# Kernel optimization log

Hardware: AMD Instinct MI355X
Metric: run time of the kernel (lower is better)

The kernel has to match this reference:

```python
import jax, jax.numpy as jnp
import numpy as np

NEG_INF = -1.0e9  # matches the -1e9 mask constant in the torch module


def setup_inputs() -> dict:
    key = jax.random.key(0)
    k1, k2, k3, k4, k5 = jax.random.split(key, 5)
    B, S, D = 8, 2048, 1024
    x = jax.random.normal(k1, (B, S, D), dtype=jnp.float32)
    mask = jax.random.randint(k2, (B, S), 0, 2, dtype=jnp.int32)
    # torch.nn.Linear stores weight as [out_features, in_features]
    scale = 1.0 / np.sqrt(D)
    w_q = jax.random.normal(k3, (D, D), dtype=jnp.float32) * scale
    w_k = jax.random.normal(k4, (D, D), dtype=jnp.float32) * scale
    w_v = jax.random.normal(k5, (D, D), dtype=jnp.float32) * scale
    return {"x": x, "mask": mask, "w_q": w_q, "w_k": w_k, "w_v": w_v}


def reference(x, mask, w_q, w_k, w_v):
    # Linear (no bias): y = x @ W^T
    q = jnp.einsum("bsd,ed->bse", x, w_q)
    k = jnp.einsum("bsd,ed->bse", x, w_k)
    v = jnp.einsum("bsd,ed->bse", x, w_v)
    # raw (unscaled) scores, exactly as in the torch module
    s = jnp.einsum("bqd,bkd->bqk", q, k)  # [B, S, S]
    # dropout p=0.0 -> identity (eval mode); mask added AFTER dropout
    s = s + NEG_INF * mask.astype(s.dtype)[:, None, :]  # broadcast over query dim
    s = jax.nn.softmax(s, axis=-1)
    out = jnp.einsum("bqk,bkd->bqd", s, v)
    return out, s
```

## Files before the change

kernel.cpp:

```cpp
#include <hip/hip_runtime.h>

#define NEG_INF_F (-1.0e9f)

typedef _Float16 f16x8 __attribute__((ext_vector_type(8)));
typedef float f32x4 __attribute__((ext_vector_type(4)));

__device__ inline unsigned short f16_of(float f) {
    _Float16 h = (_Float16)f;
    return __builtin_bit_cast(unsigned short, h);
}
__device__ inline float f32_of(unsigned short u) {
    return (float)__builtin_bit_cast(_Float16, u);
}

__device__ inline void gload16(const unsigned short* g, unsigned short* l) {
    __builtin_amdgcn_global_load_lds(
        (const __attribute__((address_space(1))) unsigned int*)g,
        (__attribute__((address_space(3))) unsigned int*)l, 16, 0, 0);
}

__device__ inline f16x8 frag32(const unsigned short* t, int r, int ch) {
    return *reinterpret_cast<const f16x8*>(&t[r * 32 + (ch ^ ((r >> 1) & 3)) * 8]);
}
__device__ inline f16x8 frag64(const unsigned short* t, int r, int ch) {
    return *reinterpret_cast<const f16x8*>(&t[r * 64 + (ch ^ (r & 7)) * 8]);
}

__device__ inline void stage_256x32(const unsigned short* __restrict__ g0, int ldg, int k0,
                                    unsigned short* qbuf, int w, int lane) {
#pragma unroll
    for (int c = 0; c < 2; ++c) {
        const int r = c * 128 + w * 16 + (lane >> 2);
        const int co = ((lane & 3) ^ ((r >> 1) & 3)) * 8;
        gload16(g0 + (long long)r * ldg + k0 + co, qbuf + (c * 128 + w * 16) * 32);
    }
}
__device__ inline void stage_128x32(const unsigned short* __restrict__ g0, int ldg, int k0,
                                    unsigned short* qbuf, int w, int lane) {
    const int r = w * 16 + (lane >> 2);
    const int co = ((lane & 3) ^ ((r >> 1) & 3)) * 8;
    gload16(g0 + (long long)r * ldg + k0 + co, qbuf + (w * 16) * 32);
}

template <int OMODE>
__global__ __launch_bounds__(512, 2) void gemm2(
    const unsigned short* __restrict__ Ah_g, const unsigned short* __restrict__ Al_g,
    long long strideA, int lda,
    const unsigned short* __restrict__ Bh_g, long long strideB, int ldb,
    unsigned short* __restrict__ Ch, long long strideC, int ldc, int K)
{
    constexpr int BUF = 16384;
    const int gx = gridDim.x, gy = gridDim.y;
    int bid = blockIdx.x + gx * (blockIdx.y + gy * blockIdx.z);
    const int nwg = gx * gy * gridDim.z;
    bid = (bid & 7) * (nwg >> 3) + (bid >> 3);
    const int bx = bid % gx;
    const int by = (bid / gx) % gy;
    const int b  = bid / (gx * gy);

    const int tid = threadIdx.x;
    const int w = tid >> 6, lane = tid & 63;
    const int wr = w & 1, wc = w >> 1;
    const int lr = lane & 15, lg = lane >> 4;
    const int rowBase = bx * 128;
    const int colBase = by * 256;

    __shared__ unsigned short smem[32768];

    const unsigned short* Ah0 = Ah_g + (long long)b * strideA + (long long)rowBase * lda;
    const unsigned short* Al0 = Al_g + (long long)b * strideA + (long long)rowBase * lda;
    const unsigned short* Bh0 = Bh_g + (long long)b * strideB + (long long)colBase * ldb;

    f32x4 acc[4][4] = {};
    const int NT = K / 32;

    stage_128x32(Ah0, lda, 0, smem, w, lane);
    stage_128x32(Al0, lda, 0, smem + 4096, w, lane);
    stage_256x32(Bh0, ldb, 0, smem + 8192, w, lane);
    __syncthreads();

    for (int kt = 0; kt < NT; ++kt) {
        const unsigned short* cbuf = smem + (kt & 1) * BUF;
        if (kt + 1 < NT) {
            unsigned short* nbuf = smem + ((kt + 1) & 1) * BUF;
            const int k1 = (kt + 1) * 32;
            stage_128x32(Ah0, lda, k1, nbuf, w, lane);
            stage_128x32(Al0, lda, k1, nbuf + 4096, w, lane);
            stage_256x32(Bh0, ldb, k1, nbuf + 8192, w, lane);
        }
        const unsigned short* tAh = cbuf;
        const unsigned short* tAl = cbuf + 4096;
        const unsigned short* tB  = cbuf + 8192;
        f16x8 ah[4], al[4], bh[4];
#pragma unroll
        for (int i = 0; i < 4; ++i) {
            const int r = wr * 64 + i * 16 + lr;
            ah[i] = frag32(tAh, r, lg);
            al[i] = frag32(tAl, r, lg);
        }
#pragma unroll
        for (int j = 0; j < 4; ++j)
            bh[j] = frag32(tB, wc * 64 + j * 16 + lr, lg);
#pragma unroll
        for (int i = 0; i < 4; ++i)
#pragma unroll
            for (int j = 0; j < 4; ++j) {
                f32x4 a = acc[i][j];
                a = __builtin_amdgcn_mfma_f32_16x16x32_f16(ah[i], bh[j], a, 0, 0, 0);
                a = __builtin_amdgcn_mfma_f32_16x16x32_f16(al[i], bh[j], a, 0, 0, 0);
                acc[i][j] = a;
            }
        __syncthreads();
    }

    __syncthreads();
    float* stg = reinterpret_cast<float*>(smem) + w * 2048;
    const int colg0 = colBase + wc * 64;
#pragma unroll
    for (int rnd = 0; rnd < 2; ++rnd) {
        const int rowg0 = rowBase + wr * 64 + rnd * 32;
#pragma unroll
        for (int ii = 0; ii < 2; ++ii)
#pragma unroll
            for (int j = 0; j < 4; ++j)
#pragma unroll
                for (int r2 = 0; r2 < 4; ++r2)
                    stg[(ii * 16 + lg * 4 + r2) * 64 + j * 16 + lr] = acc[rnd * 2 + ii][j][r2];

#pragma unroll
        for (int t = 0; t < 8; ++t) {
            const int idx = t * 256 + lane * 4;
            const int r = idx >> 6, c = idx & 63;
            const float4 v = *reinterpret_cast<const float4*>(&stg[idx]);
            ushort4 h;
            h.x = f16_of(v.x); h.y = f16_of(v.y);
            h.z = f16_of(v.z); h.w = f16_of(v.w);
            *reinterpret_cast<ushort4*>(
                &Ch[(long long)b * strideC + (long long)(rowg0 + r) * ldc + colg0 + c]) = h;
        }
    }
}

__device__ inline void stage_ktile1(
    const unsigned short* __restrict__ Ah0, int lda,
    const unsigned short* __restrict__ Bh0, int ldb,
    int k0, unsigned short* buf, int w, int lane)
{
#pragma unroll
    for (int c = 0; c < 4; ++c) {
        const int r = c * 64 + w * 8 + (lane >> 3);
        const int co = ((lane & 7) ^ (r & 7)) * 8;
        const int lb = (c * 64 + w * 8) * 64;
        gload16(Ah0 + (long long)r * lda + k0 + co, buf + lb);
        gload16(Bh0 + (long long)r * ldb + k0 + co, buf + 16384 + lb);
    }
}

template <int OMODE>
__global__ __launch_bounds__(512, 2) void mfma_gemm1(
    const unsigned short* __restrict__ Ah_g, long long strideA, int lda,
    const unsigned short* __restrict__ Bh_g, long long strideB, int ldb,
    float* __restrict__ Cf, unsigned short* __restrict__ Ch,
    long long strideC, int ldc, int K,
    const int* __restrict__ mask, long long strideMask)
{
    const int b = blockIdx.z;
    const int tid = threadIdx.x;
    const int w = tid >> 6, lane = tid & 63;
    const int wr = w >> 2, wc = w & 3;
    const int lr = lane & 15, lg = lane >> 4;
    const int rowBase = blockIdx.x * 256;
    const int colBase = blockIdx.y * 256;

    __shared__ unsigned short smem[65536];

    const unsigned short* Ah0 = Ah_g + (long long)b * strideA + (long long)rowBase * lda;
    const unsigned short* Bh0 = Bh_g + (long long)b * strideB + (long long)colBase * ldb;

    f32x4 acc[8][4] = {};
    const int NT = K / 64;

    stage_ktile1(Ah0, lda, Bh0, ldb, 0, smem, w, lane);
    __syncthreads();

    for (int kt = 0; kt < NT; ++kt) {
        const unsigned short* cbuf = smem + (kt & 1) * 32768;
        if (kt + 1 < NT)
            stage_ktile1(Ah0, lda, Bh0, ldb, (kt + 1) * 64,
                         smem + ((kt + 1) & 1) * 32768, w, lane);

        const unsigned short* tA = cbuf;
        const unsigned short* tB = cbuf + 16384;
        f16x8 bh[8];
#pragma unroll
        for (int j = 0; j < 4; ++j)
#pragma unroll
            for (int ks = 0; ks < 2; ++ks)
                bh[j * 2 + ks] = frag64(tB, wc * 64 + j * 16 + lr, ks * 4 + lg);
#pragma unroll
        for (int ih = 0; ih < 2; ++ih) {
            f16x8 ah[8];
#pragma unroll
            for (int f = 0; f < 4; ++f)
#pragma unroll
                for (int ks = 0; ks < 2; ++ks)
                    ah[f * 2 + ks] = frag64(tA, wr * 128 + ih * 64 + f * 16 + lr, ks * 4 + lg);
#pragma unroll
            for (int f = 0; f < 4; ++f)
#pragma unroll
                for (int j = 0; j < 4; ++j) {
                    f32x4 a = acc[ih * 4 + f][j];
                    a = __builtin_amdgcn_mfma_f32_16x16x32_f16(ah[f * 2 + 0], bh[j * 2 + 0], a, 0, 0, 0);
                    a = __builtin_amdgcn_mfma_f32_16x16x32_f16(ah[f * 2 + 1], bh[j * 2 + 1], a, 0, 0, 0);
                    acc[ih * 4 + f][j] = a;
                }
        }
        __syncthreads();
    }

    __syncthreads();
    float* stg = reinterpret_cast<float*>(smem) + w * 2048;
    const int colg0 = colBase + wc * 64;
#pragma unroll
    for (int rnd = 0; rnd < 4; ++rnd) {
        const int rowg0 = rowBase + wr * 128 + rnd * 32;
#pragma unroll
        for (int ii = 0; ii < 2; ++ii)
#pragma unroll
            for (int j = 0; j < 4; ++j)
#pragma unroll
                for (int r2 = 0; r2 < 4; ++r2)
                    stg[(ii * 16 + lg * 4 + r2) * 64 + j * 16 + lr] = acc[rnd * 2 + ii][j][r2];

        if constexpr (OMODE == 0) {
#pragma unroll
            for (int t = 0; t < 8; ++t) {
                const int idx = t * 256 + lane * 4;
                const int r = idx >> 6, c = idx & 63;
                float4 v = *reinterpret_cast<const float4*>(&stg[idx]);
                const int colg = colg0 + c;
                if (mask != nullptr) {
                    const int4 mv = *reinterpret_cast<const int4*>(
                        &mask[(long long)b * strideMask + colg]);
                    v.x += NEG_INF_F * (float)mv.x;
                    v.y += NEG_INF_F * (float)mv.y;
                    v.z += NEG_INF_F * (float)mv.z;
                    v.w += NEG_INF_F * (float)mv.w;
                }
                *reinterpret_cast<float4*>(
                    &Cf[(long long)b * strideC + (long long)(rowg0 + r) * ldc + colg]) = v;
            }
        } else {
            const int b2 = rowg0 >> 11;
            const int s0 = rowg0 & 2047;
            const int colg = colg0 + lane;
            alignas(16) unsigned short u[32];
#pragma unroll
            for (int rr = 0; rr < 32; ++rr) u[rr] = f16_of(stg[rr * 64 + lane]);
            unsigned short* vp = Ch + (long long)b2 * (1024LL * 2048)
                               + (long long)colg * 2048 + s0;
#pragma unroll
            for (int q = 0; q < 4; ++q)
                *reinterpret_cast<uint4*>(vp + q * 8) =
                    *reinterpret_cast<const uint4*>(&u[q * 8]);
        }
        __syncthreads();
    }
}

__global__ __launch_bounds__(256) void split2_kernel(
    const float* __restrict__ in, unsigned short* __restrict__ hi,
    unsigned short* __restrict__ lo, long long n)
{
    for (long long i = ((long long)blockIdx.x * 256 + threadIdx.x) * 4; i < n;
         i += (long long)gridDim.x * 256 * 4) {
        float4 v = *reinterpret_cast<const float4*>(&in[i]);
        ushort4 h, l;
        h.x = f16_of(v.x); l.x = f16_of(v.x - f32_of(h.x));
        h.y = f16_of(v.y); l.y = f16_of(v.y - f32_of(h.y));
        h.z = f16_of(v.z); l.z = f16_of(v.z - f32_of(h.z));
        h.w = f16_of(v.w); l.w = f16_of(v.w - f32_of(h.w));
        *reinterpret_cast<ushort4*>(&hi[i]) = h;
        *reinterpret_cast<ushort4*>(&lo[i]) = l;
    }
}

__global__ __launch_bounds__(256) void tsplit_kernel(
    const float* __restrict__ in, unsigned short* __restrict__ hi,
    unsigned short* __restrict__ lo, int N)
{
    __shared__ float tile[64][65];
    const int bi = blockIdx.x * 64;
    const int bj = blockIdx.y * 64;
    const int t = threadIdx.x;
    const int c4 = (t & 15) * 4;
    const int r0 = (t >> 4) * 4;
#pragma unroll
    for (int rr = 0; rr < 4; ++rr) {
        float4 v = *reinterpret_cast<const float4*>(
            &in[(long long)(bi + r0 + rr) * N + bj + c4]);
        tile[r0 + rr][c4 + 0] = v.x;
        tile[r0 + rr][c4 + 1] = v.y;
        tile[r0 + rr][c4 + 2] = v.z;
        tile[r0 + rr][c4 + 3] = v.w;
    }
    __syncthreads();
    const int oc  = t >> 2;
    const int or0 = (t & 3) * 16;
    alignas(16) unsigned short uh[16], ul[16];
#pragma unroll
    for (int e = 0; e < 16; ++e) {
        const float f = tile[or0 + e][oc];
        const unsigned short h = f16_of(f);
        uh[e] = h;
        ul[e] = f16_of(f - f32_of(h));
    }
    unsigned short* hp = hi + (long long)(bj + oc) * N + bi + or0;
    unsigned short* lp = lo + (long long)(bj + oc) * N + bi + or0;
    *reinterpret_cast<uint4*>(hp)     = *reinterpret_cast<const uint4*>(&uh[0]);
    *reinterpret_cast<uint4*>(hp + 8) = *reinterpret_cast<const uint4*>(&uh[8]);
    *reinterpret_cast<uint4*>(lp)     = *reinterpret_cast<const uint4*>(&ul[0]);
    *reinterpret_cast<uint4*>(lp + 8) = *reinterpret_cast<const uint4*>(&ul[8]);
}

__global__ __launch_bounds__(256) void cvt_kernel(
    const float* __restrict__ in, unsigned short* __restrict__ out, long long n)
{
    for (long long i = ((long long)blockIdx.x * 256 + threadIdx.x) * 4; i < n;
         i += (long long)gridDim.x * 256 * 4) {
        float4 v = *reinterpret_cast<const float4*>(&in[i]);
        ushort4 h;
        h.x = f16_of(v.x); h.y = f16_of(v.y); h.z = f16_of(v.z); h.w = f16_of(v.w);
        *reinterpret_cast<ushort4*>(&out[i]) = h;
    }
}

__global__ __launch_bounds__(256) void softmax_kernel(
    float* __restrict__ s, unsigned short* __restrict__ p)
{
    const long long row = blockIdx.x;
    float* sp = s + row * 2048;
    const int tid = threadIdx.x;

    float v[8];
    *reinterpret_cast<float4*>(&v[0]) = *reinterpret_cast<const float4*>(&sp[tid * 8]);
    *reinterpret_cast<float4*>(&v[4]) = *reinterpret_cast<const float4*>(&sp[tid * 8 + 4]);

    float m = v[0];
#pragma unroll
    for (int i = 1; i < 8; ++i) m = fmaxf(m, v[i]);
#pragma unroll
    for (int off = 1; off < 64; off <<= 1) m = fmaxf(m, __shfl_xor(m, off));

    __shared__ float redm[4];
    __shared__ float reds[4];
    if ((tid & 63) == 0) redm[tid >> 6] = m;
    __syncthreads();
    m = fmaxf(fmaxf(redm[0], redm[1]), fmaxf(redm[2], redm[3]));

    float sum = 0.f;
#pragma unroll
    for (int i = 0; i < 8; ++i) {
        v[i] = __expf(v[i] - m);
        sum += v[i];
    }
#pragma unroll
    for (int off = 1; off < 64; off <<= 1) sum += __shfl_xor(sum, off);
    if ((tid & 63) == 0) reds[tid >> 6] = sum;
    __syncthreads();
    sum = reds[0] + reds[1] + reds[2] + reds[3];

    const float inv = 1.0f / sum;
#pragma unroll
    for (int i = 0; i < 8; ++i) v[i] *= inv;

    *reinterpret_cast<float4*>(&sp[tid * 8])     = *reinterpret_cast<const float4*>(&v[0]);
    *reinterpret_cast<float4*>(&sp[tid * 8 + 4]) = *reinterpret_cast<const float4*>(&v[4]);

    ushort4 o0, o1;
    o0.x = f16_of(v[0]); o0.y = f16_of(v[1]); o0.z = f16_of(v[2]); o0.w = f16_of(v[3]);
    o1.x = f16_of(v[4]); o1.y = f16_of(v[5]); o1.z = f16_of(v[6]); o1.w = f16_of(v[7]);
    *reinterpret_cast<ushort4*>(&p[row * 2048 + tid * 8])     = o0;
    *reinterpret_cast<ushort4*>(&p[row * 2048 + tid * 8 + 4]) = o1;
}

extern "C" void kernel_launch(void* const* d_in, const int* in_sizes, int n_in,
                              void* d_out, int out_size, void* d_ws, size_t ws_size,
                              hipStream_t stream)
{
    (void)in_sizes; (void)n_in; (void)out_size; (void)ws_size;

    const int S = 2048, D = 1024;
    const long long BS  = 8LL * S;
    const long long SD  = (long long)S * D;
    const long long SS  = (long long)S * S;
    const long long BSD = BS * D;
    const long long DD  = (long long)D * D;

    const float* x    = (const float*)d_in[0];
    const int*   mask = (const int*)d_in[1];
    const float* wq   = (const float*)d_in[2];
    const float* wk   = (const float*)d_in[3];
    const float* wv   = (const float*)d_in[4];

    float* out = (float*)d_out;
    float* s   = out + BSD;

    unsigned short* G   = (unsigned short*)d_ws;
    unsigned short* p   = G;
    unsigned short* Vt  = G + 2 * BSD;
    unsigned short* wvh = G + 3 * BSD;
    unsigned short* Mth = wvh + DD;

    unsigned short* xh = (unsigned short*)out;
    unsigned short* xl = xh + BSD;
    unsigned short* wqTh = (unsigned short*)s;
    unsigned short* wqTl = wqTh + DD;
    unsigned short* wkTh = wqTl + DD;
    unsigned short* wkTl = wkTh + DD;

    dim3 blk256(256), blk512(512);

    split2_kernel<<<dim3(2048), blk256, 0, stream>>>(x, xh, xl, BSD);
    tsplit_kernel<<<dim3(16, 16), blk256, 0, stream>>>(wq, wqTh, wqTl, D);
    tsplit_kernel<<<dim3(16, 16), blk256, 0, stream>>>(wk, wkTh, wkTl, D);

    gemm2<2><<<dim3(8, 4, 1), blk512, 0, stream>>>(
        wkTh, wkTl, 0, D, wqTh, 0, D, Mth, 0, D, D);

    gemm2<2><<<dim3(128, 4, 1), blk512, 0, stream>>>(
        xh, xl, 0, D, Mth, 0, D, G, 0, D, D);

    mfma_gemm1<0><<<dim3(8, 8, 8), blk512, 0, stream>>>(
        G, SD, D, xh, SD, D,
        s, nullptr, SS, S, D, mask, S);

    softmax_kernel<<<dim3(16384), blk256, 0, stream>>>(s, p);

    cvt_kernel<<<dim3(512), blk256, 0, stream>>>(wv, wvh, DD);
    mfma_gemm1<3><<<dim3(64, 4, 1), blk512, 0, stream>>>(
        xh, 0, D, wvh, 0, D, nullptr, Vt, 0, D, D, nullptr, 0);

    mfma_gemm1<0><<<dim3(8, 4, 8), blk512, 0, stream>>>(
        p, SS, S, Vt, SD, S, out, nullptr, SD, D, S, nullptr, 0);
}
```

Baseline: 379.1 us.

## Fuse x·M and V projections into one GEMM, drop lo-part split of x

The x·(Wk^T Wq) projection and the V projection become a single mfma_gemm1 launch over a concatenated [M; Wv] weight with N=2048. The first half writes G row-major and the second half writes V transposed. The x low-part (xl) split and the two-term compensated gemm2 over x are removed, so x is converted to f16 only once. This cuts one launch, a full read of x, and the xl write and read. The trade-off is lower precision in the G = x·M product, since the x residual term is dropped.

```diff
diff --git a/kernel.cpp b/kernel.cpp
--- a/kernel.cpp
+++ b/kernel.cpp
@@ -42,34 +42,25 @@
     gload16(g0 + (long long)r * ldg + k0 + co, qbuf + (w * 16) * 32);
 }
 
-template <int OMODE>
 __global__ __launch_bounds__(512, 2) void gemm2(
     const unsigned short* __restrict__ Ah_g, const unsigned short* __restrict__ Al_g,
-    long long strideA, int lda,
-    const unsigned short* __restrict__ Bh_g, long long strideB, int ldb,
-    unsigned short* __restrict__ Ch, long long strideC, int ldc, int K)
+    int lda,
+    const unsigned short* __restrict__ Bh_g, int ldb,
+    unsigned short* __restrict__ Ch, int ldc, int K)
 {
     constexpr int BUF = 16384;
-    const int gx = gridDim.x, gy = gridDim.y;
-    int bid = blockIdx.x + gx * (blockIdx.y + gy * blockIdx.z);
-    const int nwg = gx * gy * gridDim.z;
-    bid = (bid & 7) * (nwg >> 3) + (bid >> 3);
-    const int bx = bid % gx;
-    const int by = (bid / gx) % gy;
-    const int b  = bid / (gx * gy);
-
     const int tid = threadIdx.x;
     const int w = tid >> 6, lane = tid & 63;
     const int wr = w & 1, wc = w >> 1;
     const int lr = lane & 15, lg = lane >> 4;
-    const int rowBase = bx * 128;
-    const int colBase = by * 256;
+    const int rowBase = blockIdx.x * 128;
+    const int colBase = blockIdx.y * 256;
 
     __shared__ unsigned short smem[32768];
 
-    const unsigned short* Ah0 = Ah_g + (long long)b * strideA + (long long)rowBase * lda;
-    const unsigned short* Al0 = Al_g + (long long)b * strideA + (long long)rowBase * lda;
-    const unsigned short* Bh0 = Bh_g + (long long)b * strideB + (long long)colBase * ldb;
+    const unsigned short* Ah0 = Ah_g + (long long)rowBase * lda;
+    const unsigned short* Al0 = Al_g + (long long)rowBase * lda;
+    const unsigned short* Bh0 = Bh_g + (long long)colBase * ldb;
 
     f32x4 acc[4][4] = {};
     const int NT = K / 32;
@@ -136,7 +127,7 @@
             h.x = f16_of(v.x); h.y = f16_of(v.y);
             h.z = f16_of(v.z); h.w = f16_of(v.w);
             *reinterpret_cast<ushort4*>(
-                &Ch[(long long)b * strideC + (long long)(rowg0 + r) * ldc + colg0 + c]) = h;
+                &Ch[(long long)(rowg0 + r) * ldc + colg0 + c]) = h;
         }
     }
 }
@@ -160,7 +151,7 @@
 __global__ __launch_bounds__(512, 2) void mfma_gemm1(
     const unsigned short* __restrict__ Ah_g, long long strideA, int lda,
     const unsigned short* __restrict__ Bh_g, long long strideB, int ldb,
-    float* __restrict__ Cf, unsigned short* __restrict__ Ch,
+    float* __restrict__ Cf, unsigned short* __restrict__ Ch, unsigned short* __restrict__ Ch2,
     long long strideC, int ldc, int K,
     const int* __restrict__ mask, long long strideMask)
 {
@@ -251,37 +242,46 @@
                     &Cf[(long long)b * strideC + (long long)(rowg0 + r) * ldc + colg]) = v;
             }
         } else {
-            const int b2 = rowg0 >> 11;
-            const int s0 = rowg0 & 2047;
-            const int colg = colg0 + lane;
-            alignas(16) unsigned short u[32];
-#pragma unroll
-            for (int rr = 0; rr < 32; ++rr) u[rr] = f16_of(stg[rr * 64 + lane]);
-            unsigned short* vp = Ch + (long long)b2 * (1024LL * 2048)
-                               + (long long)colg * 2048 + s0;
-#pragma unroll
-            for (int q = 0; q < 4; ++q)
-                *reinterpret_cast<uint4*>(vp + q * 8) =
-                    *reinterpret_cast<const uint4*>(&u[q * 8]);
+            if (colBase < 1024) {
+#pragma unroll
+                for (int t = 0; t < 8; ++t) {
+                    const int idx = t * 256 + lane * 4;
+                    const int r = idx >> 6, c = idx & 63;
+                    const float4 v = *reinterpret_cast<const float4*>(&stg[idx]);
+                    ushort4 h;
+                    h.x = f16_of(v.x); h.y = f16_of(v.y);
+                    h.z = f16_of(v.z); h.w = f16_of(v.w);
+                    *reinterpret_cast<ushort4*>(
+                        &Ch[(long long)(rowg0 + r) * ldc + colg0 + c]) = h;
+                }
+            } else {
+                const int b2 = rowg0 >> 11;
+                const int s0 = rowg0 & 2047;
+                const int vcol = colg0 - 1024 + lane;
+                alignas(16) unsigned short u[32];
+#pragma unroll
+                for (int rr = 0; rr < 32; ++rr) u[rr] = f16_of(stg[rr * 64 + lane]);
+                unsigned short* vp = Ch2 + (long long)b2 * (1024LL * 2048)
+                                   + (long long)vcol * 2048 + s0;
+#pragma unroll
+                for (int q = 0; q < 4; ++q)
+                    *reinterpret_cast<uint4*>(vp + q * 8) =
+                        *reinterpret_cast<const uint4*>(&u[q * 8]);
+            }
         }
         __syncthreads();
     }
 }
 
-__global__ __launch_bounds__(256) void split2_kernel(
-    const float* __restrict__ in, unsigned short* __restrict__ hi,
-    unsigned short* __restrict__ lo, long long n)
+__global__ __launch_bounds__(256) void cvt_kernel(
+    const float* __restrict__ in, unsigned short* __restrict__ out, long long n)
 {
     for (long long i = ((long long)blockIdx.x * 256 + threadIdx.x) * 4; i < n;
          i += (long long)gridDim.x * 256 * 4) {
         float4 v = *reinterpret_cast<const float4*>(&in[i]);
-        ushort4 h, l;
-        h.x = f16_of(v.x); l.x = f16_of(v.x - f32_of(h.x));
-        h.y = f16_of(v.y); l.y = f16_of(v.y - f32_of(h.y));
-        h.z = f16_of(v.z); l.z = f16_of(v.z - f32_of(h.z));
-        h.w = f16_of(v.w); l.w = f16_of(v.w - f32_of(h.w));
-        *reinterpret_cast<ushort4*>(&hi[i]) = h;
-        *reinterpret_cast<ushort4*>(&lo[i]) = l;
+        ushort4 h;
+        h.x = f16_of(v.x); h.y = f16_of(v.y); h.z = f16_of(v.z); h.w = f16_of(v.w);
+        *reinterpret_cast<ushort4*>(&out[i]) = h;
     }
 }
 
@@ -323,18 +323,6 @@
     *reinterpret_cast<uint4*>(lp + 8) = *reinterpret_cast<const uint4*>(&ul[8]);
 }
 
-__global__ __launch_bounds__(256) void cvt_kernel(
-    const float* __restrict__ in, unsigned short* __restrict__ out, long long n)
-{
-    for (long long i = ((long long)blockIdx.x * 256 + threadIdx.x) * 4; i < n;
-         i += (long long)gridDim.x * 256 * 4) {
-        float4 v = *reinterpret_cast<const float4*>(&in[i]);
-        ushort4 h;
-        h.x = f16_of(v.x); h.y = f16_of(v.y); h.z = f16_of(v.z); h.w = f16_of(v.w);
-        *reinterpret_cast<ushort4*>(&out[i]) = h;
-    }
-}
-
 __global__ __launch_bounds__(256) void softmax_kernel(
     float* __restrict__ s, unsigned short* __restrict__ p)
 {
@@ -406,14 +394,14 @@
     float* out = (float*)d_out;
     float* s   = out + BSD;
 
-    unsigned short* G   = (unsigned short*)d_ws;
-    unsigned short* p   = G;
-    unsigned short* Vt  = G + 2 * BSD;
-    unsigned short* wvh = G + 3 * BSD;
-    unsigned short* Mth = wvh + DD;
+    unsigned short* G    = (unsigned short*)d_ws;
+    unsigned short* p    = G;
+    unsigned short* Vt   = G + 2 * BSD;
+    unsigned short* MtWv = G + 3 * BSD;
+    unsigned short* Mth  = MtWv;
+    unsigned short* wvh  = MtWv + DD;
 
     unsigned short* xh = (unsigned short*)out;
-    unsigned short* xl = xh + BSD;
     unsigned short* wqTh = (unsigned short*)s;
     unsigned short* wqTl = wqTh + DD;
     unsigned short* wkTh = wqTl + DD;
@@ -421,26 +409,24 @@
 
     dim3 blk256(256), blk512(512);
 
-    split2_kernel<<<dim3(2048), blk256, 0, stream>>>(x, xh, xl, BSD);
+    cvt_kernel<<<dim3(4096), blk256, 0, stream>>>(x, xh, BSD);
     tsplit_kernel<<<dim3(16, 16), blk256, 0, stream>>>(wq, wqTh, wqTl, D);
     tsplit_kernel<<<dim3(16, 16), blk256, 0, stream>>>(wk, wkTh, wkTl, D);
-
-    gemm2<2><<<dim3(8, 4, 1), blk512, 0, stream>>>(
-        wkTh, wkTl, 0, D, wqTh, 0, D, Mth, 0, D, D);
-
-    gemm2<2><<<dim3(128, 4, 1), blk512, 0, stream>>>(
-        xh, xl, 0, D, Mth, 0, D, G, 0, D, D);
+    cvt_kernel<<<dim3(512), blk256, 0, stream>>>(wv, wvh, DD);
+
+    gemm2<<<dim3(8, 4, 1), blk512, 0, stream>>>(
+        wkTh, wkTl, D, wqTh, D, Mth, D, D);
+
+    mfma_gemm1<4><<<dim3(64, 8, 1), blk512, 0, stream>>>(
+        xh, 0, D, MtWv, 0, D,
+        nullptr, G, Vt, 0, D, D, nullptr, 0);
 
     mfma_gemm1<0><<<dim3(8, 8, 8), blk512, 0, stream>>>(
         G, SD, D, xh, SD, D,
-        s, nullptr, SS, S, D, mask, S);
+        s, nullptr, nullptr, SS, S, D, mask, S);
 
     softmax_kernel<<<dim3(16384), blk256, 0, stream>>>(s, p);
 
-    cvt_kernel<<<dim3(512), blk256, 0, stream>>>(wv, wvh, DD);
-    mfma_gemm1<3><<<dim3(64, 4, 1), blk512, 0, stream>>>(
-        xh, 0, D, wvh, 0, D, nullptr, Vt, 0, D, D, nullptr, 0);
-
     mfma_gemm1<0><<<dim3(8, 4, 8), blk512, 0, stream>>>(
-        p, SS, S, Vt, SD, S, out, nullptr, SD, D, S, nullptr, 0);
-}
+        p, SS, S, Vt, SD, S, out, nullptr, nullptr, SD, D, S, nullptr, 0);
+}
```

Result: faster. 322.3 us (-15.0%).
